# Performance work log

Hardware: AMD Instinct MI355X
Metric: run time of the kernel (lower is better)

Reference implementation:

```python
import jax, jax.numpy as jnp
import numpy as np

B, N = 16, 512          # graphs, nodes per graph (equal-size dynamic batch)
IN, HID, OUT, K = 256, 128, 256, 16  # hidden = in_dim // red_factor
EPS = 1e-5


def setup_inputs() -> dict:
    key = jax.random.key(0)
    ks = jax.random.split(key, 12)
    def lin(k, fi, fo):
        return jax.random.normal(k, (fi, fo), jnp.float32) / np.sqrt(fi).astype(np.float32)
    return {
        "obj_encs": jax.random.normal(ks[0], (B * N, IN), jnp.float32),
        "n_nodes": jnp.full((B,), N, dtype=jnp.int32),
        # self-graph-attention params (in -> hidden), with residual projection
        "Wq": lin(ks[1], IN, HID), "bq": jnp.zeros((HID,), jnp.float32),
        "Wk": lin(ks[2], IN, HID), "bk": jnp.zeros((HID,), jnp.float32),
        "Wv": lin(ks[3], IN, HID), "bv": jnp.zeros((HID,), jnp.float32),
        "Wr": lin(ks[4], IN, HID), "br": jnp.zeros((HID,), jnp.float32),
        # EdgeConv (local+global => 2*HID input features)
        "Wc": lin(ks[5], 2 * HID, OUT), "bc": jnp.zeros((OUT,), jnp.float32),
        # LayerNorm affine
        "ln_scale": jnp.ones((OUT,), jnp.float32),
        "ln_bias": jnp.zeros((OUT,), jnp.float32),
    }


def _forward(obj_encs, n_nodes, Wq, bq, Wk, bk, Wv, bv, Wr, br, Wc, bc, ln_scale, ln_bias):
    # dynamic batching: equal-size graphs per n_nodes -> reshape [B, N, IN]
    x = obj_encs.reshape(B, N, IN)

    # --- SelfGraphAttentionLinear (per-graph dot-product attention, residual) ---
    q = x @ Wq + bq                      # [B, N, HID]
    kk = x @ Wk + bk
    v = x @ Wv + bv
    attn = jax.nn.softmax(jnp.einsum('bnd,bmd->bnm', q, kk) / np.sqrt(HID).astype(np.float32), axis=-1)
    h = jnp.einsum('bnm,bmd->bnd', attn, v) + (x @ Wr + br)  # residual projection

    # --- GraphConv: kNN (euclidean) within each graph ---
    sq = jnp.sum(h * h, axis=-1)                             # [B, N]
    dist = sq[:, :, None] + sq[:, None, :] - 2.0 * jnp.einsum('bnd,bmd->bnm', h, h)
    _, idx = jax.lax.top_k(-dist, K)                         # [B, N, K] (self included)

    nb = jax.vmap(lambda hb, ib: hb[ib])(h, idx)             # [B, N, K, HID]
    hc = h[:, :, None, :]                                    # [B, N, 1, HID]
    # features='local+global': [x_i, x_j - x_i]
    e = jnp.concatenate([jnp.broadcast_to(hc, nb.shape), nb - hc], axis=-1)  # [B,N,K,2H]

    y = jnp.einsum('bnkf,fo->bnko', e, Wc) + bc              # [B, N, K, OUT]
    y = jnp.max(y, axis=2)                                   # reduction='max' over k

    mu = jnp.mean(y, axis=-1, keepdims=True)
    var = jnp.mean((y - mu) ** 2, axis=-1, keepdims=True)
    y = (y - mu) / jnp.sqrt(var + EPS) * ln_scale + ln_bias  # LayerNorm
    return jax.nn.selu(y).reshape(B * N, OUT)


def reference(obj_encs, n_nodes, Wq, bq, Wk, bk, Wv, bv, Wr, br, Wc, bc, ln_scale, ln_bias):
    return _forward(obj_encs, n_nodes, Wq, bq, Wk, bk, Wv, bv, Wr, br, Wc, bc, ln_scale, ln_bias)
```

## Files before the change

kernel.cpp:

```cpp
#include <hip/hip_runtime.h>
#include <math.h>

#define NB   16
#define NN   512
#define FIN  256
#define HID  128
#define FOUT 256
#define TOPK 16
#define ROWS (NB*NN)
#define LN_EPS 1e-5f

#define BK   32
#define LDK  40
#define NTHR 256

typedef __attribute__((ext_vector_type(8)))  short  bf16x8;
typedef __attribute__((ext_vector_type(4)))  float  f32x4;
typedef __attribute__((ext_vector_type(8)))  unsigned short u16x8;

#define MFMA3(d, ah, al, bh, bl)                                              \
    d = __builtin_amdgcn_mfma_f32_16x16x32_bf16(ah, bh, d, 0, 0, 0);          \
    d = __builtin_amdgcn_mfma_f32_16x16x32_bf16(ah, bl, d, 0, 0, 0);          \
    d = __builtin_amdgcn_mfma_f32_16x16x32_bf16(al, bh, d, 0, 0, 0);

__device__ __forceinline__ ushort f2bf_rn(float x) {
    uint u = __float_as_uint(x);
    u += 0x7fff + ((u >> 16) & 1);
    return (ushort)(u >> 16);
}
__device__ __forceinline__ float bf2f(ushort h) {
    return __uint_as_float(((uint)h) << 16);
}
__device__ __forceinline__ void split2(float x, ushort& hi, ushort& lo) {
    hi = f2bf_rn(x);
    lo = f2bf_rn(x - bf2f(hi));
}

__device__ __forceinline__ void stage_rows64f(ushort (*Dh)[LDK], ushort (*Dl)[LDK],
                                              const float* __restrict__ src,
                                              int rstride, int tid)
{
    const int r = tid >> 2, seg = (tid & 3) * 8;
    const float* p = src + (size_t)r * rstride + seg;
    #pragma unroll
    for (int i = 0; i < 2; i++) {
        const float4 q = *(const float4*)(p + 4*i);
        ushort h0,l0,h1,l1,h2,l2,h3,l3;
        split2(q.x,h0,l0); split2(q.y,h1,l1);
        split2(q.z,h2,l2); split2(q.w,h3,l3);
        *(ushort4*)&Dh[r][seg + 4*i] = make_ushort4(h0,h1,h2,h3);
        *(ushort4*)&Dl[r][seg + 4*i] = make_ushort4(l0,l1,l2,l3);
    }
}

__device__ __forceinline__ void stage_cols64f(ushort (*Dh)[LDK], ushort (*Dl)[LDK],
                                              const float* __restrict__ src,
                                              int ldn, int tid)
{
    const int n = tid & 63, kh = (tid >> 6) * 8;
    const float* p = src + (size_t)kh * ldn + n;
    ushort hh[8], ll[8];
    #pragma unroll
    for (int i = 0; i < 8; i++) split2(p[(size_t)i * ldn], hh[i], ll[i]);
    *(ushort4*)&Dh[n][kh]     = make_ushort4(hh[0],hh[1],hh[2],hh[3]);
    *(ushort4*)&Dh[n][kh + 4] = make_ushort4(hh[4],hh[5],hh[6],hh[7]);
    *(ushort4*)&Dl[n][kh]     = make_ushort4(ll[0],ll[1],ll[2],ll[3]);
    *(ushort4*)&Dl[n][kh + 4] = make_ushort4(ll[4],ll[5],ll[6],ll[7]);
}

__device__ __forceinline__ void stage_u(ushort (*Ds)[LDK], const ushort* __restrict__ src,
                                        int rstride, int tid)
{
    const int r = tid >> 2, seg = (tid & 3) * 8;
    *(u16x8*)&Ds[r][seg] = *(const u16x8*)(src + (size_t)r * rstride + seg);
}

__device__ __forceinline__ void mma_step64(const ushort (*Ah)[LDK], const ushort (*Al)[LDK],
                                           const ushort (*Bh)[LDK], const ushort (*Bl)[LDK],
                                           f32x4 acc[2][2], int wr, int wc, int lane)
{
    const int q8 = (lane >> 4) * 8, m = lane & 15;
    bf16x8 ah[2], al[2], bh[2], bl[2];
    #pragma unroll
    for (int i = 0; i < 2; i++) {
        ah[i] = *(const bf16x8*)&Ah[wr + 16*i + m][q8];
        al[i] = *(const bf16x8*)&Al[wr + 16*i + m][q8];
        bh[i] = *(const bf16x8*)&Bh[wc + 16*i + m][q8];
        bl[i] = *(const bf16x8*)&Bl[wc + 16*i + m][q8];
    }
    #pragma unroll
    for (int i = 0; i < 2; i++)
        #pragma unroll
        for (int j = 0; j < 2; j++) {
            MFMA3(acc[i][j], ah[i], al[i], bh[j], bl[j]);
        }
}

struct Params {
    const float *X, *Wq, *bq, *Wk, *bk, *Wv, *bv, *Wr, *br, *Wc, *bc, *lns, *lnb;
    float *out;
    float *Rbuf, *SQ, *AB, *D, *Opart, *Lpart;
    ushort *Yh, *Yl, *Vth, *Vtl, *Hh, *Hl, *Wcth, *Wctl;
};

__global__ __launch_bounds__(NTHR, 2) void k_pA(Params P)
{
    __shared__ ushort SMEM[4*64*LDK];

    const int tid = threadIdx.x;

    if (blockIdx.x >= 1024) {
        float (*fb)[65] = (float(*)[65])SMEM;
        const int n0 = (blockIdx.x - 1024) * 64;
        const bool ahalf = n0 < 256;
        const int cbase = n0 & 255;
        for (int kt = 0; kt < 2; kt++) {
            const int k0 = kt * 64;
            __syncthreads();
            {
                const int kk = tid >> 2, cs = (tid & 3) * 16;
                #pragma unroll
                for (int t = 0; t < 16; t++) {
                    const float bot = P.Wc[(size_t)(HID + k0 + kk)*FOUT + cbase + cs + t];
                    float val = bot;
                    if (ahalf) val = P.Wc[(size_t)(k0 + kk)*FOUT + cbase + cs + t] - bot;
                    fb[kk][cs+t] = val;
                }
            }
            __syncthreads();
            {
                const int c = tid >> 2, ks = (tid & 3) * 16;
                u16x8 vh0, vh1, vl0, vl1;
                #pragma unroll
                for (int t = 0; t < 8; t++) {
                    ushort hh, ll;
                    split2(fb[ks+t][c], hh, ll);   vh0[t]=hh; vl0[t]=ll;
                    split2(fb[ks+8+t][c], hh, ll); vh1[t]=hh; vl1[t]=ll;
                }
                *(u16x8*)&P.Wcth[(size_t)(n0+c)*128 + k0 + ks]     = vh0;
                *(u16x8*)&P.Wcth[(size_t)(n0+c)*128 + k0 + ks + 8] = vh1;
                *(u16x8*)&P.Wctl[(size_t)(n0+c)*128 + k0 + ks]     = vl0;
                *(u16x8*)&P.Wctl[(size_t)(n0+c)*128 + k0 + ks + 8] = vl1;
            }
        }
        return;
    }

    ushort (*Ah)[LDK] = (ushort(*)[LDK])(SMEM);
    ushort (*Al)[LDK] = (ushort(*)[LDK])(SMEM + 2560);
    ushort (*Bh)[LDK] = (ushort(*)[LDK])(SMEM + 5120);
    ushort (*Bl)[LDK] = (ushort(*)[LDK])(SMEM + 7680);
    float* fbuf = (float*)SMEM;

    const int lane = tid & 63, w = tid >> 6;
    const int wr = (w >> 1) * 32, wc = (w & 1) * 32;
    const int m = lane & 15, q4 = (lane >> 4) * 4;

    const int job = blockIdx.x;
    const int ct = job >> 7, br0 = (job & 127) * 64;
    const int widx = ct >> 1, ch = (ct & 1) * 64;
    const float* W    = widx==0 ? P.Wq : widx==1 ? P.Wk : widx==2 ? P.Wv : P.Wr;
    const float* bias = widx==0 ? P.bq : widx==1 ? P.bk : widx==2 ? P.bv : P.br;

    f32x4 acc[2][2];
    #pragma unroll
    for (int i = 0; i < 2; i++)
        #pragma unroll
        for (int j = 0; j < 2; j++) acc[i][j] = (f32x4){0.f,0.f,0.f,0.f};

    for (int k0 = 0; k0 < FIN; k0 += BK) {
        stage_rows64f(Ah, Al, P.X + (size_t)br0 * FIN + k0, FIN, tid);
        stage_cols64f(Bh, Bl, W + (size_t)k0 * HID + ch, HID, tid);
        __syncthreads();
        mma_step64(Ah, Al, Bh, Bl, acc, wr, wc, lane);
        __syncthreads();
    }
    #pragma unroll
    for (int i = 0; i < 2; i++)
        #pragma unroll
        for (int reg = 0; reg < 4; reg++) {
            const int r = wr + 16*i + q4 + reg;
            #pragma unroll
            for (int j = 0; j < 2; j++) {
                const int c = wc + 16*j + m;
                fbuf[r*65 + c] = acc[i][j][reg] + bias[ch + c];
            }
        }
    __syncthreads();

    if (ct < 4) {
        const float qsc = (ct < 2) ? 0.08838834764831845f : 1.0f;
        const int r = tid >> 2, cs = (tid & 3) * 16;
        u16x8 vh0, vh1, vl0, vl1;
        #pragma unroll
        for (int t = 0; t < 8; t++) {
            ushort hh, ll;
            split2(fbuf[r*65 + cs + t] * qsc, hh, ll);     vh0[t]=hh; vl0[t]=ll;
            split2(fbuf[r*65 + cs + 8 + t] * qsc, hh, ll); vh1[t]=hh; vl1[t]=ll;
        }
        const size_t o = (size_t)(br0 + r) * 256 + ct*64 + cs;
        *(u16x8*)&P.Yh[o]   = vh0; *(u16x8*)&P.Yh[o+8] = vh1;
        *(u16x8*)&P.Yl[o]   = vl0; *(u16x8*)&P.Yl[o+8] = vl1;
    } else if (ct < 6) {
        const int cl = tid >> 2, rs = (tid & 3) * 16;
        const int b = br0 >> 9, nb = br0 & 511;
        const int cglob = (ct - 4) * 64 + cl;
        u16x8 vh0, vh1, vl0, vl1;
        #pragma unroll
        for (int t = 0; t < 8; t++) {
            ushort hh, ll;
            split2(fbuf[(rs+t)*65 + cl], hh, ll);   vh0[t]=hh; vl0[t]=ll;
            split2(fbuf[(rs+8+t)*65 + cl], hh, ll); vh1[t]=hh; vl1[t]=ll;
        }
        const size_t o = ((size_t)b*128 + cglob) * 512 + nb + rs;
        *(u16x8*)&P.Vth[o]   = vh0; *(u16x8*)&P.Vth[o+8] = vh1;
        *(u16x8*)&P.Vtl[o]   = vl0; *(u16x8*)&P.Vtl[o+8] = vl1;
    } else {
        const int r = tid >> 2, cs = (tid & 3) * 16;
        float* dst = P.Rbuf + (size_t)(br0 + r) * 128 + (ct - 6)*64 + cs;
        #pragma unroll
        for (int t = 0; t < 16; t += 4) {
            float4 q;
            q.x = fbuf[r*65+cs+t];   q.y = fbuf[r*65+cs+t+1];
            q.z = fbuf[r*65+cs+t+2]; q.w = fbuf[r*65+cs+t+3];
            *(float4*)(dst + t) = q;
        }
    }
}

__global__ __launch_bounds__(NTHR, 2) void k_pB(Params P)
{
    __shared__ ushort SMEM[4*64*LDK];
    ushort (*P0h)[LDK] = (ushort(*)[LDK])(SMEM);
    ushort (*P0l)[LDK] = (ushort(*)[LDK])(SMEM + 2560);
    ushort (*Bh)[LDK]  = (ushort(*)[LDK])(SMEM + 5120);
    ushort (*Bl)[LDK]  = (ushort(*)[LDK])(SMEM + 7680);

    const int tid = threadIdx.x, lane = tid & 63, w = tid >> 6;
    const int L = lane & 15, quad = lane >> 4;

    const int job = blockIdx.x;
    const int b = job >> 6, rest = job & 63;
    const int n0 = (rest >> 3) * 64, mc = rest & 7, m0 = mc * 64;
    const int grow0 = b*NN + n0 + w*16;

    bf16x8 qh[4], ql[4];
    #pragma unroll
    for (int s = 0; s < 4; s++) {
        const size_t qo = (size_t)(grow0 + L) * 256 + s*32 + quad*8;
        qh[s] = *(const bf16x8*)(P.Yh + qo);
        ql[s] = *(const bf16x8*)(P.Yl + qo);
    }

    f32x4 Sf[4];
    #pragma unroll
    for (int j = 0; j < 4; j++) Sf[j] = (f32x4){0.f,0.f,0.f,0.f};

    for (int s = 0; s < 4; s++) {
        __syncthreads();
        {
            const int r = tid >> 2, seg = (tid & 3) * 8;
            const size_t o = (size_t)(b*NN + m0 + r) * 256 + 128 + s*32 + seg;
            *(u16x8*)&Bh[r][seg] = *(const u16x8*)(P.Yh + o);
            *(u16x8*)&Bl[r][seg] = *(const u16x8*)(P.Yl + o);
        }
        __syncthreads();
        #pragma unroll
        for (int j = 0; j < 4; j++) {
            bf16x8 kh = *(const bf16x8*)&Bh[16*j + L][quad*8];
            bf16x8 kl = *(const bf16x8*)&Bl[16*j + L][quad*8];
            MFMA3(Sf[j], qh[s], ql[s], kh, kl);
        }
    }

    __syncthreads();

    float ls[4] = {0.f, 0.f, 0.f, 0.f};
    #pragma unroll
    for (int j = 0; j < 4; j++)
        #pragma unroll
        for (int r = 0; r < 4; r++) {
            const float p = __expf(Sf[j][r]);
            ls[r] += p;
            const int row = w*16 + quad*4 + r, cc = (16*j + L) & 31;
            ushort hh, ll; split2(p, hh, ll);
            if (j < 2) { P0h[row][cc] = hh; P0l[row][cc] = ll; }
            else       { Bh[row][cc]  = hh; Bl[row][cc]  = ll; }
        }
    #pragma unroll
    for (int r = 0; r < 4; r++) {
        float v = ls[r];
        v += __shfl_xor(v, 1); v += __shfl_xor(v, 2);
        v += __shfl_xor(v, 4); v += __shfl_xor(v, 8);
        ls[r] = v;
    }

    f32x4 O[8];
    #pragma unroll
    for (int j = 0; j < 8; j++) O[j] = (f32x4){0.f,0.f,0.f,0.f};
    #pragma unroll
    for (int s2 = 0; s2 < 2; s2++) {
        bf16x8 ph = s2 ? *(const bf16x8*)&Bh[w*16 + L][quad*8]
                       : *(const bf16x8*)&P0h[w*16 + L][quad*8];
        bf16x8 pl = s2 ? *(const bf16x8*)&Bl[w*16 + L][quad*8]
                       : *(const bf16x8*)&P0l[w*16 + L][quad*8];
        #pragma unroll
        for (int j = 0; j < 8; j++) {
            const size_t vo = ((size_t)(b*128 + 16*j + L)) * 512 + m0 + s2*32 + quad*8;
            bf16x8 vh = *(const bf16x8*)(P.Vth + vo);
            bf16x8 vl = *(const bf16x8*)(P.Vtl + vo);
            MFMA3(O[j], ph, pl, vh, vl);
        }
    }

    #pragma unroll
    for (int j = 0; j < 8; j++)
        #pragma unroll
        for (int reg = 0; reg < 4; reg++) {
            const int grow = grow0 + quad*4 + reg;
            P.Opart[((size_t)mc*ROWS + grow)*128 + 16*j + L] = O[j][reg];
        }
    if (L == 0) {
        #pragma unroll
        for (int reg = 0; reg < 4; reg++)
            P.Lpart[(size_t)mc*ROWS + grow0 + quad*4 + reg] = ls[reg];
    }
}

__global__ __launch_bounds__(NTHR, 2) void k_pC(Params P)
{
    const int lane = threadIdx.x & 63, w = threadIdx.x >> 6;
    const int row = blockIdx.x * 4 + w;
    float Ls = 0.f, o0 = 0.f, o1 = 0.f;
    #pragma unroll
    for (int p = 0; p < 8; p++) {
        Ls += P.Lpart[(size_t)p*ROWS + row];
        const float* op = P.Opart + ((size_t)p*ROWS + row)*128;
        o0 += op[lane];
        o1 += op[lane + 64];
    }
    const float invl = 1.0f / Ls;
    const float h0 = o0*invl + P.Rbuf[(size_t)row*128 + lane];
    const float h1 = o1*invl + P.Rbuf[(size_t)row*128 + lane + 64];
    ushort hh, ll;
    split2(h0, hh, ll); P.Hh[(size_t)row*128 + lane] = hh;      P.Hl[(size_t)row*128 + lane] = ll;
    split2(h1, hh, ll); P.Hh[(size_t)row*128 + lane + 64] = hh; P.Hl[(size_t)row*128 + lane + 64] = ll;
    float s = h0*h0 + h1*h1;
    #pragma unroll
    for (int off = 1; off < 64; off <<= 1) s += __shfl_xor(s, off);
    if (lane == 0) P.SQ[row] = s;
}

__global__ __launch_bounds__(NTHR, 2) void k_pD(Params P)
{
    __shared__ ushort SMEM[4*64*LDK];
    ushort (*Ah)[LDK] = (ushort(*)[LDK])(SMEM);
    ushort (*Al)[LDK] = (ushort(*)[LDK])(SMEM + 2560);
    ushort (*Bh)[LDK] = (ushort(*)[LDK])(SMEM + 5120);
    ushort (*Bl)[LDK] = (ushort(*)[LDK])(SMEM + 7680);

    const int tid = threadIdx.x, lane = tid & 63, w = tid >> 6;
    const int wr = (w >> 1) * 32, wc = (w & 1) * 32;
    const int m = lane & 15, q4 = (lane >> 4) * 4;
    const int job = blockIdx.x;

    f32x4 acc[2][2];
    #pragma unroll
    for (int i = 0; i < 2; i++)
        #pragma unroll
        for (int j = 0; j < 2; j++) acc[i][j] = (f32x4){0.f,0.f,0.f,0.f};

    if (job < 1024) {
        const int ct = job >> 7, br0 = (job & 127) * 64;
        const bool bhalf = ct >= 4;
        const int c0 = (ct & 3) * 64;
        for (int k0 = 0; k0 < HID; k0 += BK) {
            stage_u(Ah, P.Hh + (size_t)br0 * 128 + k0, 128, tid);
            stage_u(Al, P.Hl + (size_t)br0 * 128 + k0, 128, tid);
            stage_u(Bh, P.Wcth + (size_t)(ct*64) * 128 + k0, 128, tid);
            stage_u(Bl, P.Wctl + (size_t)(ct*64) * 128 + k0, 128, tid);
            __syncthreads();
            mma_step64(Ah, Al, Bh, Bl, acc, wr, wc, lane);
            __syncthreads();
        }
        #pragma unroll
        for (int i = 0; i < 2; i++)
            #pragma unroll
            for (int reg = 0; reg < 4; reg++) {
                const int grow = br0 + wr + 16*i + q4 + reg;
                #pragma unroll
                for (int j = 0; j < 2; j++) {
                    const int c = wc + 16*j + m;
                    const float add = bhalf ? 0.0f : P.bc[c0 + c];
                    P.AB[(size_t)grow * 512 + ct*64 + c] = acc[i][j][reg] + add;
                }
            }
    } else {
        const int t = job - 1024;
        const int b = t >> 6, rest = t & 63;
        const int m0 = (rest >> 3) * 64, n0 = (rest & 7) * 64;
        for (int k0 = 0; k0 < HID; k0 += BK) {
            stage_u(Ah, P.Hh + (size_t)(b*NN + n0) * 128 + k0, 128, tid);
            stage_u(Al, P.Hl + (size_t)(b*NN + n0) * 128 + k0, 128, tid);
            stage_u(Bh, P.Hh + (size_t)(b*NN + m0) * 128 + k0, 128, tid);
            stage_u(Bl, P.Hl + (size_t)(b*NN + m0) * 128 + k0, 128, tid);
            __syncthreads();
            mma_step64(Ah, Al, Bh, Bl, acc, wr, wc, lane);
            __syncthreads();
        }
        const int gb = b * NN;
        float* Db = P.D + (size_t)b * NN * NN;
        float sqm[2];
        #pragma unroll
        for (int j = 0; j < 2; j++) sqm[j] = P.SQ[gb + m0 + wc + 16*j + m];
        #pragma unroll
        for (int i = 0; i < 2; i++)
            #pragma unroll
            for (int reg = 0; reg < 4; reg++) {
                const int n = n0 + wr + 16*i + q4 + reg;
                const float sqn = P.SQ[gb + n];
                #pragma unroll
                for (int j = 0; j < 2; j++)
                    Db[(size_t)n * NN + m0 + wc + 16*j + m]
                        = sqn + sqm[j] - 2.0f * acc[i][j][reg];
            }
    }
}

__global__ __launch_bounds__(NTHR, 2) void k_pE(Params P)
{
    const int lane = threadIdx.x & 63, w = threadIdx.x >> 6;
    const int row = blockIdx.x * 4 + w;
    const int gb0 = row & ~(NN - 1);
    const float* drow = P.D + (size_t)row * NN;
    const float4 dq0 = ((const float4*)drow)[lane];
    const float4 dq1 = ((const float4*)drow)[64 + lane];
    float v[8] = {dq0.x, dq0.y, dq0.z, dq0.w, dq1.x, dq1.y, dq1.z, dq1.w};

    const float lsc0 = P.lns[lane],       lbi0 = P.lnb[lane];
    const float lsc1 = P.lns[lane + 64],  lbi1 = P.lnb[lane + 64];
    const float lsc2 = P.lns[lane + 128], lbi2 = P.lnb[lane + 128];
    const float lsc3 = P.lns[lane + 192], lbi3 = P.lnb[lane + 192];
    const float* arow = P.AB + (size_t)row * 512;
    const float a0 = arow[lane], a1 = arow[lane + 64],
                a2 = arow[lane + 128], a3 = arow[lane + 192];

    float bm0 = -INFINITY, bm1 = -INFINITY, bm2 = -INFINITY, bm3 = -INFINITY;

    for (int it = 0; it < TOPK; it++) {
        float bestv = v[0]; int bestm = 4*lane;
        #pragma unroll
        for (int j = 1; j < 8; j++) {
            const int mm = (j >> 2)*256 + 4*lane + (j & 3);
            if (v[j] < bestv) { bestv = v[j]; bestm = mm; }
        }
        #pragma unroll
        for (int off = 1; off < 64; off <<= 1) {
            const float ov = __shfl_xor(bestv, off);
            const int   om = __shfl_xor(bestm, off);
            if (ov < bestv || (ov == bestv && om < bestm)) { bestv = ov; bestm = om; }
        }
        const float* brow = P.AB + (size_t)(gb0 + bestm) * 512 + 256;
        bm0 = fmaxf(bm0, brow[lane]);
        bm1 = fmaxf(bm1, brow[lane + 64]);
        bm2 = fmaxf(bm2, brow[lane + 128]);
        bm3 = fmaxf(bm3, brow[lane + 192]);
        if (((bestm >> 2) & 63) == lane) {
            const int jj = ((bestm >> 8) << 2) | (bestm & 3);
            #pragma unroll
            for (int j = 0; j < 8; j++) if (j == jj) v[j] = INFINITY;
        }
    }

    float y0 = a0 + bm0, y1 = a1 + bm1, y2 = a2 + bm2, y3 = a3 + bm3;
    float s = y0 + y1 + y2 + y3;
    #pragma unroll
    for (int off = 1; off < 64; off <<= 1) s += __shfl_xor(s, off);
    const float mu = s * (1.0f/256.0f);
    const float d0 = y0 - mu, d1 = y1 - mu, d2 = y2 - mu, d3 = y3 - mu;
    float s2 = d0*d0 + d1*d1 + d2*d2 + d3*d3;
    #pragma unroll
    for (int off = 1; off < 64; off <<= 1) s2 += __shfl_xor(s2, off);
    const float var = s2 * (1.0f/256.0f);
    const float rstd = rsqrtf(var + LN_EPS);

    const float lam = 1.0507009873554805f, alpha = 1.6732632423543772f;
    float* orow = P.out + (size_t)row * FOUT;
    { const float z = d0*rstd*lsc0 + lbi0; orow[lane]       = z > 0.f ? lam*z : lam*alpha*expm1f(z); }
    { const float z = d1*rstd*lsc1 + lbi1; orow[lane + 64]  = z > 0.f ? lam*z : lam*alpha*expm1f(z); }
    { const float z = d2*rstd*lsc2 + lbi2; orow[lane + 128] = z > 0.f ? lam*z : lam*alpha*expm1f(z); }
    { const float z = d3*rstd*lsc3 + lbi3; orow[lane + 192] = z > 0.f ? lam*z : lam*alpha*expm1f(z); }
}

extern "C" void kernel_launch(void* const* d_in, const int* in_sizes, int n_in,
                              void* d_out, int out_size, void* d_ws, size_t ws_size,
                              hipStream_t stream)
{
    (void)in_sizes; (void)n_in; (void)out_size; (void)ws_size;

    char* cur = (char*)d_ws;
    auto alloc = [&](size_t bytes) { char* p = cur; cur += (bytes + 255) & ~size_t(255); return p; };

    Params P;
    P.X   = (const float*)d_in[0];
    P.Wq  = (const float*)d_in[2];
    P.bq  = (const float*)d_in[3];
    P.Wk  = (const float*)d_in[4];
    P.bk  = (const float*)d_in[5];
    P.Wv  = (const float*)d_in[6];
    P.bv  = (const float*)d_in[7];
    P.Wr  = (const float*)d_in[8];
    P.br  = (const float*)d_in[9];
    P.Wc  = (const float*)d_in[10];
    P.bc  = (const float*)d_in[11];
    P.lns = (const float*)d_in[12];
    P.lnb = (const float*)d_in[13];
    P.out = (float*)d_out;

    P.D     = (float*)alloc((size_t)NB*NN*NN*4);
    P.AB    = (float*)alloc((size_t)ROWS*512*4);
    P.Opart = (float*)alloc((size_t)8*ROWS*128*4);
    P.Lpart = (float*)alloc((size_t)8*ROWS*4);
    P.Rbuf  = (float*)alloc((size_t)ROWS*128*4);
    P.SQ    = (float*)alloc((size_t)ROWS*4);
    P.Yh    = (ushort*)alloc((size_t)ROWS*256*2);
    P.Yl    = (ushort*)alloc((size_t)ROWS*256*2);
    P.Vth   = (ushort*)alloc((size_t)NB*128*512*2);
    P.Vtl   = (ushort*)alloc((size_t)NB*128*512*2);
    P.Hh    = (ushort*)alloc((size_t)ROWS*128*2);
    P.Hl    = (ushort*)alloc((size_t)ROWS*128*2);
    P.Wcth  = (ushort*)alloc((size_t)512*128*2);
    P.Wctl  = (ushort*)alloc((size_t)512*128*2);

    k_pA<<<1032, NTHR, 0, stream>>>(P);
    k_pB<<<1024, NTHR, 0, stream>>>(P);
    k_pC<<<2048, NTHR, 0, stream>>>(P);
    k_pD<<<2048, NTHR, 0, stream>>>(P);
    k_pE<<<2048, NTHR, 0, stream>>>(P);
}
```

Baseline: 183.4 us.

## Exploit distance-matrix symmetry and batch neighbor gathers after top-k selection

The pairwise distance kernel now computes only upper-triangular 64x64 tiles per graph (36 instead of 64). Each off-diagonal tile is transposed through shared memory and written to the mirrored position, which cuts the Gram-matrix MFMA work by nearly half. In the top-k kernel, the 16 neighbor indices are collected first and the AB row gathers plus the max reduction happen afterwards in an unrolled loop. That lets the loads be issued together instead of being serialized with the shuffle-based selection. The costs are extra shared-memory traffic, a barrier and strided transpose reads for the mirrored tiles, plus a small serial loop to decode the tile index.

```diff
diff --git a/kernel.cpp b/kernel.cpp
--- a/kernel.cpp
+++ b/kernel.cpp
@@ -397,8 +397,12 @@
             }
     } else {
         const int t = job - 1024;
-        const int b = t >> 6, rest = t & 63;
-        const int m0 = (rest >> 3) * 64, n0 = (rest & 7) * 64;
+        const int b = t / 36;
+        int rem = t - b * 36, ti = 0;
+        while (rem >= 8 - ti) { rem -= 8 - ti; ti++; }
+        const int tj = ti + rem;
+        const int n0 = ti * 64, m0 = tj * 64;
+
         for (int k0 = 0; k0 < HID; k0 += BK) {
             stage_u(Ah, P.Hh + (size_t)(b*NN + n0) * 128 + k0, 128, tid);
             stage_u(Al, P.Hl + (size_t)(b*NN + n0) * 128 + k0, 128, tid);
@@ -413,17 +417,37 @@
         float sqm[2];
         #pragma unroll
         for (int j = 0; j < 2; j++) sqm[j] = P.SQ[gb + m0 + wc + 16*j + m];
+
+        float* fbuf = (float*)SMEM;
         #pragma unroll
         for (int i = 0; i < 2; i++)
             #pragma unroll
             for (int reg = 0; reg < 4; reg++) {
-                const int n = n0 + wr + 16*i + q4 + reg;
+                const int rloc = wr + 16*i + q4 + reg;
+                const int n = n0 + rloc;
                 const float sqn = P.SQ[gb + n];
                 #pragma unroll
-                for (int j = 0; j < 2; j++)
-                    Db[(size_t)n * NN + m0 + wc + 16*j + m]
-                        = sqn + sqm[j] - 2.0f * acc[i][j][reg];
+                for (int j = 0; j < 2; j++) {
+                    const int cloc = wc + 16*j + m;
+                    const float val = sqn + sqm[j] - 2.0f * acc[i][j][reg];
+                    Db[(size_t)n * NN + m0 + cloc] = val;
+                    if (ti != tj) fbuf[rloc*65 + cloc] = val;
+                }
             }
+        if (ti != tj) {
+            __syncthreads();
+            const int mloc = tid >> 2, cs = (tid & 3) * 16;
+            float* dst = Db + (size_t)(m0 + mloc) * NN + n0 + cs;
+            #pragma unroll
+            for (int tt = 0; tt < 16; tt += 4) {
+                float4 q;
+                q.x = fbuf[(cs+tt)*65   + mloc];
+                q.y = fbuf[(cs+tt+1)*65 + mloc];
+                q.z = fbuf[(cs+tt+2)*65 + mloc];
+                q.w = fbuf[(cs+tt+3)*65 + mloc];
+                *(float4*)(dst + tt) = q;
+            }
+        }
     }
 }
 
@@ -445,8 +469,8 @@
     const float a0 = arow[lane], a1 = arow[lane + 64],
                 a2 = arow[lane + 128], a3 = arow[lane + 192];
 
-    float bm0 = -INFINITY, bm1 = -INFINITY, bm2 = -INFINITY, bm3 = -INFINITY;
-
+    int idx[TOPK];
+    #pragma unroll
     for (int it = 0; it < TOPK; it++) {
         float bestv = v[0]; int bestm = 4*lane;
         #pragma unroll
@@ -460,16 +484,22 @@
             const int   om = __shfl_xor(bestm, off);
             if (ov < bestv || (ov == bestv && om < bestm)) { bestv = ov; bestm = om; }
         }
-        const float* brow = P.AB + (size_t)(gb0 + bestm) * 512 + 256;
+        idx[it] = bestm;
+        if (((bestm >> 2) & 63) == lane) {
+            const int jj = ((bestm >> 8) << 2) | (bestm & 3);
+            #pragma unroll
+            for (int j = 0; j < 8; j++) if (j == jj) v[j] = INFINITY;
+        }
+    }
+
+    float bm0 = -INFINITY, bm1 = -INFINITY, bm2 = -INFINITY, bm3 = -INFINITY;
+    #pragma unroll
+    for (int k2 = 0; k2 < TOPK; k2++) {
+        const float* brow = P.AB + (size_t)(gb0 + idx[k2]) * 512 + 256;
         bm0 = fmaxf(bm0, brow[lane]);
         bm1 = fmaxf(bm1, brow[lane + 64]);
         bm2 = fmaxf(bm2, brow[lane + 128]);
         bm3 = fmaxf(bm3, brow[lane + 192]);
-        if (((bestm >> 2) & 63) == lane) {
-            const int jj = ((bestm >> 8) << 2) | (bestm & 3);
-            #pragma unroll
-            for (int j = 0; j < 8; j++) if (j == jj) v[j] = INFINITY;
-        }
     }
 
     float y0 = a0 + bm0, y1 = a1 + bm1, y2 = a2 + bm2, y3 = a3 + bm3;
@@ -535,6 +565,6 @@
     k_pA<<<1032, NTHR, 0, stream>>>(P);
     k_pB<<<1024, NTHR, 0, stream>>>(P);
     k_pC<<<2048, NTHR, 0, stream>>>(P);
-    k_pD<<<2048, NTHR, 0, stream>>>(P);
+    k_pD<<<1600, NTHR, 0, stream>>>(P);
     k_pE<<<2048, NTHR, 0, stream>>>(P);
 }
```

Result: faster. 179.7 us (-2.0%).
